# Kernel optimization log

Measured on AMD Instinct MI355X. Metric: run time of the kernel, lower is better.

## Reference

```python
import jax, jax.numpy as jnp
import numpy as np

ALPHA_LIF = 0.85   # FastLIFCell decay
V_TH = 2.0         # FastLIFCell threshold
ALPHA_LI = 0.9     # FastLICell decay


def setup_inputs() -> dict:
    key = jax.random.key(0)
    k1, k2 = jax.random.split(key)
    # [T, C=1, H, W] spiking input sequence
    x = jax.random.normal(k1, (256, 1, 512, 512), dtype=jnp.float32)
    # learned conv kernel, Conv2d(1,1,5,padding=2,bias=False) -> OIHW [1,1,5,5]
    kernel = jax.random.normal(k2, (1, 1, 5, 5), dtype=jnp.float32) * 0.2
    return {"x": x, "kernel": kernel}


def reference(x, kernel):
    # Conv weights are time-invariant: apply the SAME-padded conv to all
    # timesteps at once (T acts as the batch dim), identical math to the
    # per-step torch conv.
    pad = (kernel.shape[-1] - 1) // 2
    c = jax.lax.conv_general_dilated(
        x, kernel, window_strides=(1, 1),
        padding=[(pad, pad), (pad, pad)],
        dimension_numbers=("NCHW", "OIHW", "NCHW"),
    )  # [T, 1, H, W]

    def step(carry, c_t):
        s1, s2 = carry
        # FastLIF: leaky integrate, fire, soft reset (subtract threshold)
        v = ALPHA_LIF * s1 + c_t
        spk = (v >= V_TH).astype(v.dtype)
        s1_new = v - spk * V_TH
        # FastLI: leaky integrator readout of the spikes
        s2_new = ALPHA_LI * s2 + spk
        return (s1_new, s2_new), s2_new

    s0 = jnp.zeros(x.shape[1:], dtype=x.dtype)  # [1, H, W]
    _, out = jax.lax.scan(step, (s0, s0), c)
    return out  # [T, 1, H, W]
```

## Files before the change

### kernel.cpp

```cpp
#include <hip/hip_runtime.h>


namespace {

typedef float f32x2 __attribute__((ext_vector_type(2)));

constexpr int T_STEPS = 256;
constexpr int H = 512;
constexpr int W = 512;
constexpr int HW = H * W;
constexpr int TW = 64;
constexpr int TH = 8;
constexpr int HALO_W = TW + 4;
constexpr int HALO_H = TH + 4;
constexpr int NLOAD = HALO_W * HALO_H;
constexpr int NTHREADS = 256;

__device__ __forceinline__ void sync_nodrain_vm() {
    __builtin_amdgcn_sched_barrier(0);
    asm volatile("s_waitcnt lgkmcnt(0)");
    __builtin_amdgcn_s_barrier();
    __builtin_amdgcn_sched_barrier(0);
}

__global__ __launch_bounds__(NTHREADS, 2)
void snn_fused(const float* __restrict__ x, const float* __restrict__ kern,
               float* __restrict__ out) {
    #pragma clang fp contract(off)

    __shared__ alignas(16) float smem[2][NLOAD];

    const int tid = threadIdx.x;
    const int w0 = blockIdx.x * TW;
    const int h0 = blockIdx.y * TH;

    double wgt[25];
    #pragma unroll
    for (int i = 0; i < 25; ++i) wgt[i] = (double)kern[i];

    int  goff[4];
    bool gval[4];
    #pragma unroll
    for (int i = 0; i < 4; ++i) {
        int idx = tid + i * NTHREADS;
        int lhh = idx / HALO_W;
        int lww = idx - lhh * HALO_W;
        int gh = h0 - 2 + lhh;
        int gw = w0 - 2 + lww;
        goff[i] = gh * W + gw;
        gval[i] = (idx < NLOAD) &&
                  ((unsigned)gh < (unsigned)H) && ((unsigned)gw < (unsigned)W);
    }

    const int lwp = (tid & 31) * 2;
    const int lh  = tid >> 5;
    const int gh  = h0 + lh;
    const int gw  = w0 + lwp;

    double s1a = 0.0, s2a = 0.0;
    double s1b = 0.0, s2b = 0.0;

    float rA[4], rB[4];
    #pragma unroll
    for (int i = 0; i < 4; ++i) { rA[i] = 0.0f; rB[i] = 0.0f; }

    auto issue_loads = [&](int t, float* r) {
        const float* xt = x + (size_t)t * HW;
        #pragma unroll
        for (int i = 0; i < 4; ++i) {
            if (gval[i]) r[i] = xt[goff[i]];
        }
    };

    auto stage_write = [&](float* buf, const float* r) {
        #pragma unroll
        for (int i = 0; i < 4; ++i) {
            int idx = tid + i * NTHREADS;
            if (idx < NLOAD) buf[idx] = r[i];
        }
    };

    auto step = [&](const float* buf, int t) {
        #pragma clang fp contract(off)
        const float* sm = buf + lh * HALO_W + lwp;
        double acc0 = 0.0, acc1 = 0.0;
        #pragma unroll
        for (int kh = 0; kh < 5; ++kh) {
            const f32x2* r2 = reinterpret_cast<const f32x2*>(sm + kh * HALO_W);
            f32x2 f0 = r2[0], f1 = r2[1], f2 = r2[2];
            double c0 = (double)f0.x, c1 = (double)f0.y;
            double c2 = (double)f1.x, c3 = (double)f1.y;
            double c4 = (double)f2.x, c5 = (double)f2.y;
            acc0 = __builtin_fma(wgt[kh * 5 + 0], c0, acc0);
            acc1 = __builtin_fma(wgt[kh * 5 + 0], c1, acc1);
            acc0 = __builtin_fma(wgt[kh * 5 + 1], c1, acc0);
            acc1 = __builtin_fma(wgt[kh * 5 + 1], c2, acc1);
            acc0 = __builtin_fma(wgt[kh * 5 + 2], c2, acc0);
            acc1 = __builtin_fma(wgt[kh * 5 + 2], c3, acc1);
            acc0 = __builtin_fma(wgt[kh * 5 + 3], c3, acc0);
            acc1 = __builtin_fma(wgt[kh * 5 + 3], c4, acc1);
            acc0 = __builtin_fma(wgt[kh * 5 + 4], c4, acc0);
            acc1 = __builtin_fma(wgt[kh * 5 + 4], c5, acc1);
        }

        {
            double v = 0.85 * s1a + acc0;
            double spk = (v >= 2.0) ? 1.0 : 0.0;
            s1a = v - spk * 2.0;
            s2a = 0.9 * s2a + spk;
        }
        {
            double v = 0.85 * s1b + acc1;
            double spk = (v >= 2.0) ? 1.0 : 0.0;
            s1b = v - spk * 2.0;
            s2b = 0.9 * s2b + spk;
        }

        f32x2 o;
        o.x = (float)s2a;
        o.y = (float)s2b;
        f32x2* outp = reinterpret_cast<f32x2*>(
            out + (size_t)t * HW + (size_t)gh * W + gw);
        __builtin_nontemporal_store(o, outp);
    };

    issue_loads(0, rA);
    issue_loads(1, rB);
    stage_write(smem[0], rA);
    sync_nodrain_vm();

    for (int tb = 0; tb < 127; ++tb) {
        const int t0 = 2 * tb;

        issue_loads(t0 + 2, rA);
        step(smem[0], t0);
        stage_write(smem[1], rB);
        sync_nodrain_vm();

        issue_loads(t0 + 3, rB);
        step(smem[1], t0 + 1);
        stage_write(smem[0], rA);
        sync_nodrain_vm();
    }

    step(smem[0], 254);
    stage_write(smem[1], rB);
    sync_nodrain_vm();
    step(smem[1], 255);
}

}

extern "C" void kernel_launch(void* const* d_in, const int* in_sizes, int n_in,
                              void* d_out, int out_size, void* d_ws, size_t ws_size,
                              hipStream_t stream) {
    const float* x    = (const float*)d_in[0];
    const float* kern = (const float*)d_in[1];
    float* out        = (float*)d_out;

    dim3 grid(W / TW, H / TH);
    snn_fused<<<grid, dim3(NTHREADS), 0, stream>>>(x, kern, out);
}
```

Baseline: 541.8 us.

## Give each wave a private halo tile to drop block-wide barriers

```diff
diff --git a/kernel.cpp b/kernel.cpp
--- a/kernel.cpp
+++ b/kernel.cpp
@@ -5,88 +5,88 @@
 
 typedef float f32x2 __attribute__((ext_vector_type(2)));
 
-constexpr int T_STEPS = 256;
 constexpr int H = 512;
 constexpr int W = 512;
 constexpr int HW = H * W;
 constexpr int TW = 64;
 constexpr int TH = 8;
-constexpr int HALO_W = TW + 4;
-constexpr int HALO_H = TH + 4;
-constexpr int NLOAD = HALO_W * HALO_H;
+constexpr int WAVE_ROWS = 2;
+constexpr int WHALO_W = TW + 4;
+constexpr int WHALO_H = WAVE_ROWS + 4;
+constexpr int WNLOAD = WHALO_W * WHALO_H;
+constexpr int NSLOT = 7;
 constexpr int NTHREADS = 256;
-
-__device__ __forceinline__ void sync_nodrain_vm() {
-    __builtin_amdgcn_sched_barrier(0);
-    asm volatile("s_waitcnt lgkmcnt(0)");
-    __builtin_amdgcn_s_barrier();
-    __builtin_amdgcn_sched_barrier(0);
-}
+constexpr int NWAVES = NTHREADS / 64;
 
 __global__ __launch_bounds__(NTHREADS, 2)
 void snn_fused(const float* __restrict__ x, const float* __restrict__ kern,
                float* __restrict__ out) {
     #pragma clang fp contract(off)
 
-    __shared__ alignas(16) float smem[2][NLOAD];
+    __shared__ alignas(16) float smem[NWAVES][2][WNLOAD];
 
-    const int tid = threadIdx.x;
-    const int w0 = blockIdx.x * TW;
-    const int h0 = blockIdx.y * TH;
+    const int tid  = threadIdx.x;
+    const int lane = tid & 63;
+    const int wv   = tid >> 6;
+    const int w0   = blockIdx.x * TW;
+    const int h0   = blockIdx.y * TH + wv * WAVE_ROWS;
 
     double wgt[25];
     #pragma unroll
     for (int i = 0; i < 25; ++i) wgt[i] = (double)kern[i];
 
-    int  goff[4];
-    bool gval[4];
+    int  goff[NSLOT];
+    bool gval[NSLOT];
     #pragma unroll
-    for (int i = 0; i < 4; ++i) {
-        int idx = tid + i * NTHREADS;
-        int lhh = idx / HALO_W;
-        int lww = idx - lhh * HALO_W;
-        int gh = h0 - 2 + lhh;
-        int gw = w0 - 2 + lww;
+    for (int i = 0; i < NSLOT; ++i) {
+        int idx = lane + i * 64;
+        int hr  = idx / WHALO_W;
+        int hc  = idx - hr * WHALO_W;
+        int gh  = h0 - 2 + hr;
+        int gw  = w0 - 2 + hc;
         goff[i] = gh * W + gw;
-        gval[i] = (idx < NLOAD) &&
+        gval[i] = (idx < WNLOAD) &&
                   ((unsigned)gh < (unsigned)H) && ((unsigned)gw < (unsigned)W);
     }
 
-    const int lwp = (tid & 31) * 2;
-    const int lh  = tid >> 5;
-    const int gh  = h0 + lh;
-    const int gw  = w0 + lwp;
+    const int lh  = lane >> 5;
+    const int lwp = (lane & 31) * 2;
+    const int ghh = h0 + lh;
+    const int gww = w0 + lwp;
 
     double s1a = 0.0, s2a = 0.0;
     double s1b = 0.0, s2b = 0.0;
 
-    float rA[4], rB[4];
+    float rA[NSLOT], rB[NSLOT];
     #pragma unroll
-    for (int i = 0; i < 4; ++i) { rA[i] = 0.0f; rB[i] = 0.0f; }
+    for (int i = 0; i < NSLOT; ++i) { rA[i] = 0.0f; rB[i] = 0.0f; }
+
+    float* bufA = &smem[wv][0][0];
+    float* bufB = &smem[wv][1][0];
 
     auto issue_loads = [&](int t, float* r) {
         const float* xt = x + (size_t)t * HW;
         #pragma unroll
-        for (int i = 0; i < 4; ++i) {
+        for (int i = 0; i < NSLOT; ++i) {
             if (gval[i]) r[i] = xt[goff[i]];
         }
     };
 
     auto stage_write = [&](float* buf, const float* r) {
         #pragma unroll
-        for (int i = 0; i < 4; ++i) {
-            int idx = tid + i * NTHREADS;
-            if (idx < NLOAD) buf[idx] = r[i];
+        for (int i = 0; i < NSLOT; ++i) {
+            int idx = lane + i * 64;
+            if (idx < WNLOAD) buf[idx] = r[i];
         }
     };
 
     auto step = [&](const float* buf, int t) {
         #pragma clang fp contract(off)
-        const float* sm = buf + lh * HALO_W + lwp;
+        const float* sm = buf + lh * WHALO_W + lwp;
         double acc0 = 0.0, acc1 = 0.0;
         #pragma unroll
         for (int kh = 0; kh < 5; ++kh) {
-            const f32x2* r2 = reinterpret_cast<const f32x2*>(sm + kh * HALO_W);
+            const f32x2* r2 = reinterpret_cast<const f32x2*>(sm + kh * WHALO_W);
             f32x2 f0 = r2[0], f1 = r2[1], f2 = r2[2];
             double c0 = (double)f0.x, c1 = (double)f0.y;
             double c2 = (double)f1.x, c3 = (double)f1.y;
@@ -120,33 +120,29 @@
         o.x = (float)s2a;
         o.y = (float)s2b;
         f32x2* outp = reinterpret_cast<f32x2*>(
-            out + (size_t)t * HW + (size_t)gh * W + gw);
+            out + (size_t)t * HW + (size_t)ghh * W + gww);
         __builtin_nontemporal_store(o, outp);
     };
 
     issue_loads(0, rA);
     issue_loads(1, rB);
-    stage_write(smem[0], rA);
-    sync_nodrain_vm();
+    stage_write(bufA, rA);
 
     for (int tb = 0; tb < 127; ++tb) {
         const int t0 = 2 * tb;
 
         issue_loads(t0 + 2, rA);
-        step(smem[0], t0);
-        stage_write(smem[1], rB);
-        sync_nodrain_vm();
+        step(bufA, t0);
+        stage_write(bufB, rB);
 
         issue_loads(t0 + 3, rB);
-        step(smem[1], t0 + 1);
-        stage_write(smem[0], rA);
-        sync_nodrain_vm();
+        step(bufB, t0 + 1);
+        stage_write(bufA, rA);
     }
 
-    step(smem[0], 254);
-    stage_write(smem[1], rB);
-    sync_nodrain_vm();
-    step(smem[1], 255);
+    step(bufA, 254);
+    stage_write(bufB, rB);
+    step(bufB, 255);
 }
 
 }
```

Result: no change. 548.1 us (+1.2%).

## Switch to one pixel per thread with shorter tiles and higher occupancy

Applied to the files above, without the earlier changes.

```diff
diff --git a/kernel.cpp b/kernel.cpp
--- a/kernel.cpp
+++ b/kernel.cpp
@@ -3,18 +3,18 @@
 
 namespace {
 
-typedef float f32x2 __attribute__((ext_vector_type(2)));
+struct __attribute__((packed, aligned(4))) fpair { float a, b; };
 
-constexpr int T_STEPS = 256;
 constexpr int H = 512;
 constexpr int W = 512;
 constexpr int HW = H * W;
 constexpr int TW = 64;
-constexpr int TH = 8;
+constexpr int TH = 4;
 constexpr int HALO_W = TW + 4;
 constexpr int HALO_H = TH + 4;
 constexpr int NLOAD = HALO_W * HALO_H;
 constexpr int NTHREADS = 256;
+constexpr int NSLOT = 3;
 
 __device__ __forceinline__ void sync_nodrain_vm() {
     __builtin_amdgcn_sched_barrier(0);
@@ -23,7 +23,7 @@
     __builtin_amdgcn_sched_barrier(0);
 }
 
-__global__ __launch_bounds__(NTHREADS, 2)
+__global__ __launch_bounds__(NTHREADS, 4)
 void snn_fused(const float* __restrict__ x, const float* __restrict__ kern,
                float* __restrict__ out) {
     #pragma clang fp contract(off)
@@ -38,10 +38,10 @@
     #pragma unroll
     for (int i = 0; i < 25; ++i) wgt[i] = (double)kern[i];
 
-    int  goff[4];
-    bool gval[4];
+    int  goff[NSLOT];
+    bool gval[NSLOT];
     #pragma unroll
-    for (int i = 0; i < 4; ++i) {
+    for (int i = 0; i < NSLOT; ++i) {
         int idx = tid + i * NTHREADS;
         int lhh = idx / HALO_W;
         int lww = idx - lhh * HALO_W;
@@ -52,29 +52,28 @@
                   ((unsigned)gh < (unsigned)H) && ((unsigned)gw < (unsigned)W);
     }
 
-    const int lwp = (tid & 31) * 2;
-    const int lh  = tid >> 5;
-    const int gh  = h0 + lh;
-    const int gw  = w0 + lwp;
+    const int lw = tid & 63;
+    const int lh = tid >> 6;
+    const int gh = h0 + lh;
+    const int gw = w0 + lw;
 
-    double s1a = 0.0, s2a = 0.0;
-    double s1b = 0.0, s2b = 0.0;
+    double s1 = 0.0, s2 = 0.0;
 
-    float rA[4], rB[4];
+    float rA[NSLOT], rB[NSLOT];
     #pragma unroll
-    for (int i = 0; i < 4; ++i) { rA[i] = 0.0f; rB[i] = 0.0f; }
+    for (int i = 0; i < NSLOT; ++i) { rA[i] = 0.0f; rB[i] = 0.0f; }
 
     auto issue_loads = [&](int t, float* r) {
         const float* xt = x + (size_t)t * HW;
         #pragma unroll
-        for (int i = 0; i < 4; ++i) {
+        for (int i = 0; i < NSLOT; ++i) {
             if (gval[i]) r[i] = xt[goff[i]];
         }
     };
 
     auto stage_write = [&](float* buf, const float* r) {
         #pragma unroll
-        for (int i = 0; i < 4; ++i) {
+        for (int i = 0; i < NSLOT; ++i) {
             int idx = tid + i * NTHREADS;
             if (idx < NLOAD) buf[idx] = r[i];
         }
@@ -82,46 +81,31 @@
 
     auto step = [&](const float* buf, int t) {
         #pragma clang fp contract(off)
-        const float* sm = buf + lh * HALO_W + lwp;
-        double acc0 = 0.0, acc1 = 0.0;
+        const float* sm = buf + lh * HALO_W + lw;
+        double acc = 0.0;
         #pragma unroll
         for (int kh = 0; kh < 5; ++kh) {
-            const f32x2* r2 = reinterpret_cast<const f32x2*>(sm + kh * HALO_W);
-            f32x2 f0 = r2[0], f1 = r2[1], f2 = r2[2];
-            double c0 = (double)f0.x, c1 = (double)f0.y;
-            double c2 = (double)f1.x, c3 = (double)f1.y;
-            double c4 = (double)f2.x, c5 = (double)f2.y;
-            acc0 = __builtin_fma(wgt[kh * 5 + 0], c0, acc0);
-            acc1 = __builtin_fma(wgt[kh * 5 + 0], c1, acc1);
-            acc0 = __builtin_fma(wgt[kh * 5 + 1], c1, acc0);
-            acc1 = __builtin_fma(wgt[kh * 5 + 1], c2, acc1);
-            acc0 = __builtin_fma(wgt[kh * 5 + 2], c2, acc0);
-            acc1 = __builtin_fma(wgt[kh * 5 + 2], c3, acc1);
-            acc0 = __builtin_fma(wgt[kh * 5 + 3], c3, acc0);
-            acc1 = __builtin_fma(wgt[kh * 5 + 3], c4, acc1);
-            acc0 = __builtin_fma(wgt[kh * 5 + 4], c4, acc0);
-            acc1 = __builtin_fma(wgt[kh * 5 + 4], c5, acc1);
+            const float* row = sm + kh * HALO_W;
+            fpair p01 = *reinterpret_cast<const fpair*>(row);
+            fpair p23 = *reinterpret_cast<const fpair*>(row + 2);
+            float c4f = row[4];
+            double c0 = (double)p01.a, c1 = (double)p01.b;
+            double c2 = (double)p23.a, c3 = (double)p23.b;
+            double c4 = (double)c4f;
+            acc = __builtin_fma(wgt[kh * 5 + 0], c0, acc);
+            acc = __builtin_fma(wgt[kh * 5 + 1], c1, acc);
+            acc = __builtin_fma(wgt[kh * 5 + 2], c2, acc);
+            acc = __builtin_fma(wgt[kh * 5 + 3], c3, acc);
+            acc = __builtin_fma(wgt[kh * 5 + 4], c4, acc);
         }
 
-        {
-            double v = 0.85 * s1a + acc0;
-            double spk = (v >= 2.0) ? 1.0 : 0.0;
-            s1a = v - spk * 2.0;
-            s2a = 0.9 * s2a + spk;
-        }
-        {
-            double v = 0.85 * s1b + acc1;
-            double spk = (v >= 2.0) ? 1.0 : 0.0;
-            s1b = v - spk * 2.0;
-            s2b = 0.9 * s2b + spk;
-        }
+        double v = 0.85 * s1 + acc;
+        double spk = (v >= 2.0) ? 1.0 : 0.0;
+        s1 = v - spk * 2.0;
+        s2 = 0.9 * s2 + spk;
 
-        f32x2 o;
-        o.x = (float)s2a;
-        o.y = (float)s2b;
-        f32x2* outp = reinterpret_cast<f32x2*>(
-            out + (size_t)t * HW + (size_t)gh * W + gw);
-        __builtin_nontemporal_store(o, outp);
+        float* outp = out + (size_t)t * HW + (size_t)gh * W + gw;
+        __builtin_nontemporal_store((float)s2, outp);
     };
 
     issue_loads(0, rA);
```

After: 538.6 us. No clear change (-0.6%).
